# Performance work log

Measured on AMD Instinct MI355X. Metric: run time of the kernel, lower is better.

Reference implementation:

```python
import jax, jax.numpy as jnp
import numpy as np

B = 64
SIZES = [5023, 1256, 314, 79, 20]
NV = [s + 1 for s in SIZES]          # vertex counts incl. padding vertex
K = 12                               # spiral length (all levels)
LAT = 128
ENC_F = [3, 16, 32, 64, 128]
DEC_IN = [128, 64, 32, 32, 16]
DEC_OUT = [64, 32, 32, 16, 3]


def setup_inputs() -> dict:
    keys = iter(jax.random.split(jax.random.key(0), 80))

    def nrm(shape, scale=1.0):
        return jax.random.normal(next(keys), shape, jnp.float32) * scale

    inp = {}
    inp['x_talking'] = nrm((B, NV[0], 3))
    inp['template'] = nrm((B, NV[0], 3))
    for i in range(4):
        inp['D%d' % i] = nrm((NV[i + 1], NV[i]), 1.0 / np.sqrt(NV[i]))
        inp['U%d' % i] = nrm((NV[i], NV[i + 1]), 1.0 / np.sqrt(NV[i + 1]))
    for i in range(4):
        fan = ENC_F[i] * K
        inp['enc_w%d' % i] = nrm((ENC_F[i + 1], fan), 1.0 / np.sqrt(fan))
        inp['enc_b%d' % i] = jnp.zeros((ENC_F[i + 1],), jnp.float32)
    inp['fc_enc_w'] = nrm((LAT, NV[4] * DEC_IN[0]), 1.0 / np.sqrt(NV[4] * DEC_IN[0]))
    inp['fc_enc_b'] = jnp.zeros((LAT,), jnp.float32)
    inp['fc_dec_w'] = nrm((NV[4] * DEC_IN[0], 2 * LAT), 1.0 / np.sqrt(2 * LAT))
    inp['fc_dec_b'] = jnp.zeros((NV[4] * DEC_IN[0],), jnp.float32)
    for i in range(5):
        fan = DEC_IN[i] * K
        inp['dec_w%d' % i] = nrm((DEC_OUT[i], fan), 1.0 / np.sqrt(fan))
        inp['dec_b%d' % i] = jnp.zeros((DEC_OUT[i],), jnp.float32)
    for i in range(4):
        inp['S%d' % i] = jax.random.randint(next(keys), (NV[i], K), 0, NV[i], jnp.int32)
    return inp


def _spiral_conv(x, S, W, b, act):
    # x: [B, N, F]; S: [N, K] spiral neighbor indices; W: [out, K*F] (torch Linear layout)
    Bv, Nv, F = x.shape
    g = x[:, S, :].reshape(Bv, Nv, K * F)            # spiral neighbor gather
    y = act(jnp.einsum('bnf,of->bno', g, W) + b)     # gather-GEMM + activation
    mask = jnp.ones((1, Nv, 1), y.dtype).at[0, -1, 0].set(0.0)  # zero out padding vertex
    return y * mask


def _forward(x_talking, template, D, U, enc, fc_enc_w, fc_enc_b, fc_dec_w, fc_dec_b, dec, S):
    elu = jax.nn.elu
    # encode_talking
    x = x_talking
    for i in range(4):
        x = _spiral_conv(x, S[i], enc[i][0], enc[i][1], elu)
        x = jnp.einsum('mn,bnf->bmf', D[i], x)       # downsample
    z = x.reshape(B, -1) @ fc_enc_w.T + fc_enc_b     # [B, latent]
    # decode(z, z)
    h = jnp.concatenate([z, z], axis=1) @ fc_dec_w.T + fc_dec_b
    x = h.reshape(B, NV[4], DEC_IN[0])
    for i in range(3):
        x = jnp.einsum('mn,bnf->bmf', U[3 - i], x)   # upsample
        x = _spiral_conv(x, S[3 - i], dec[i][0], dec[i][1], elu)
    x = jnp.einsum('mn,bnf->bmf', U[0], x)
    x = _spiral_conv(x, S[0], dec[3][0], dec[3][1], elu)
    x = _spiral_conv(x, S[0], dec[4][0], dec[4][1], lambda v: v)  # identity activation
    return x, x + template


def reference(x_talking, template, D0, D1, D2, D3, U0, U1, U2, U3,
              enc_w0, enc_b0, enc_w1, enc_b1, enc_w2, enc_b2, enc_w3, enc_b3,
              fc_enc_w, fc_enc_b, fc_dec_w, fc_dec_b,
              dec_w0, dec_b0, dec_w1, dec_b1, dec_w2, dec_b2, dec_w3, dec_b3, dec_w4, dec_b4,
              S0, S1, S2, S3):
    return _forward(
        x_talking, template,
        [D0, D1, D2, D3], [U0, U1, U2, U3],
        [(enc_w0, enc_b0), (enc_w1, enc_b1), (enc_w2, enc_b2), (enc_w3, enc_b3)],
        fc_enc_w, fc_enc_b, fc_dec_w, fc_dec_b,
        [(dec_w0, dec_b0), (dec_w1, dec_b1), (dec_w2, dec_b2), (dec_w3, dec_b3), (dec_w4, dec_b4)],
        [S0, S1, S2, S3])
```

## Files before the change

kernel.cpp:

```cpp
#include <hip/hip_runtime.h>
#include <cstddef>


#define BATCH 64
#define SPK 12

typedef __attribute__((ext_vector_type(8))) short bf16x8;
typedef __attribute__((ext_vector_type(4))) short bf16x4;
typedef __attribute__((ext_vector_type(4))) float f32x4;

__device__ __forceinline__ unsigned short f2bf(float x) {
    union { float f; unsigned int u; } v; v.f = x;
    unsigned int r = v.u + 0x7FFF + ((v.u >> 16) & 1);
    return (unsigned short)(r >> 16);
}

__global__ __launch_bounds__(256) void f32_to_bf16_kernel(
    const float* __restrict__ in, unsigned short* __restrict__ out, int n8)
{
    int i = blockIdx.x * 256 + threadIdx.x;
    if (i < n8) {
        const float* p = in + (size_t)i * 8;
        bf16x8 r;
#pragma unroll
        for (int j = 0; j < 8; ++j) r[j] = (short)f2bf(p[j]);
        *(bf16x8*)(out + (size_t)i * 8) = r;
    }
}

__global__ __launch_bounds__(256) void reducep_bf16_kernel(
    const float* __restrict__ P, size_t ps, unsigned short* __restrict__ out,
    int n8, int nparts)
{
    int i = blockIdx.x * 256 + threadIdx.x;
    if (i < n8) {
        size_t base = (size_t)i * 8;
        bf16x8 r;
#pragma unroll
        for (int j = 0; j < 8; ++j) {
            float v = P[base + j];
            for (int p = 1; p < nparts; ++p) v += P[(size_t)p * ps + base + j];
            r[j] = (short)f2bf(v);
        }
        *(bf16x8*)(out + base) = r;
    }
}

__global__ __launch_bounds__(256) void a_bf16_pad_kernel(
    const float* __restrict__ A, unsigned short* __restrict__ Ap,
    int M, int K, int Kp, int total)
{
    int i = blockIdx.x * 256 + threadIdx.x;
    if (i >= total) return;
    int kp8 = Kp >> 3;
    int m = i / kp8;
    int k0 = (i - m * kp8) * 8;
    bf16x8 r;
    if (m < M) {
        const float* src = A + (size_t)m * K + k0;
#pragma unroll
        for (int j = 0; j < 8; ++j) {
            float v = (k0 + j < K) ? src[j] : 0.f;
            r[j] = (short)f2bf(v);
        }
    } else {
#pragma unroll
        for (int j = 0; j < 8; ++j) r[j] = 0;
    }
    *(bf16x8*)(Ap + (size_t)m * Kp + k0) = r;
}

__global__ __launch_bounds__(256) void w_frag16_kernel(
    const unsigned short* __restrict__ Wb, unsigned short* __restrict__ Wfs,
    int KF, int total)
{
    int i = blockIdx.x * 256 + threadIdx.x;
    if (i >= total) return;
    int j    = i & 7;
    int lane = (i >> 3) & 63;
    int s    = i >> 9;
    int l15  = lane & 15;
    int quad = (lane >> 4) & 3;
    Wfs[i] = Wb[l15 * KF + s * 32 + quad * 8 + j];
}

template<int LOGF, int OBF16>
__global__ __launch_bounds__(64, 4) void conv_cmfma_kernel(
    const unsigned short* __restrict__ x, const int* __restrict__ S,
    const unsigned short* __restrict__ Wfs, const float* __restrict__ bias,
    void* __restrict__ yv, int Nv, int elu_flag, int swz)
{
    constexpr int F     = 1 << LOGF;
    constexpr int KF    = SPK * F;
    constexpr int NS    = KF / 32;
    constexpr int RPADu = (LOGF == 5) ? 40 : 24;
    __shared__ unsigned short Gs[12 * 16 * RPADu];

    const int lane = threadIdx.x;
    const int l15  = lane & 15;
    const int quad = (lane >> 4) & 3;

    int bx = blockIdx.x, bz = blockIdx.z;
    if (swz) {
        const int gx = gridDim.x;
        const int total = gx * gridDim.z;
        int bid = bx + gx * bz;
        const int chunk = total >> 3;
        int sid = (bid & 7) * chunk + (bid >> 3);
        bx = sid % gx;
        bz = sid / gx;
    }
    const int n0 = bx * 16;
    const int b  = bz;
    const size_t xb = (size_t)b * Nv;

    int4 sv;
    {
        int g = lane >> 4; if (g > 2) g = 2;
        int n = n0 + l15; if (n >= Nv) n = 0;
        sv = *(const int4*)(S + n * SPK + g * 4);
    }

    if constexpr (LOGF == 5) {
        const int grow = lane >> 2, gchk = lane & 3;
#pragma unroll
        for (int k = 0; k < 12; ++k) {
            int sel = ((k >> 2) << 4) | grow;
            int comp = k & 3;
            int src = (comp == 0) ? __shfl(sv.x, sel)
                    : (comp == 1) ? __shfl(sv.y, sel)
                    : (comp == 2) ? __shfl(sv.z, sel)
                                  : __shfl(sv.w, sel);
            bf16x8 v = *(const bf16x8*)(x + ((xb + src) << 5) + gchk * 8);
            *(bf16x8*)&Gs[k * 16 * RPADu + grow * RPADu + gchk * 8] = v;
        }
    } else {
        const int khalf = lane >> 5, grow = (lane >> 1) & 15, gchk = lane & 1;
#pragma unroll
        for (int g = 0; g < 6; ++g) {
            int k0 = 2 * g;
            int sel0 = ((k0 >> 2) << 4) | grow;
            int sel1 = (((k0 + 1) >> 2) << 4) | grow;
            int s0 = ((k0 & 3) == 0) ? __shfl(sv.x, sel0) : __shfl(sv.z, sel0);
            int s1 = (((k0 + 1) & 3) == 1) ? __shfl(sv.y, sel1) : __shfl(sv.w, sel1);
            int src = khalf ? s1 : s0;
            int k   = k0 + khalf;
            bf16x8 v = *(const bf16x8*)(x + ((xb + src) << 4) + gchk * 8);
            *(bf16x8*)&Gs[k * 16 * RPADu + grow * RPADu + gchk * 8] = v;
        }
    }

    f32x4 acc0 = (f32x4){0.f, 0.f, 0.f, 0.f};
    f32x4 acc1 = (f32x4){0.f, 0.f, 0.f, 0.f};
#pragma unroll
    for (int s = 0; s < NS; ++s) {
        int kf = s * 32 + quad * 8;
        int k  = kf >> LOGF;
        int f  = kf & (F - 1);
        bf16x8 a = *(const bf16x8*)&Gs[k * 16 * RPADu + l15 * RPADu + f];
        bf16x8 w = *(const bf16x8*)(Wfs + (s * 64 + lane) * 8);
        if (s & 1) acc1 = __builtin_amdgcn_mfma_f32_16x16x32_bf16(a, w, acc1, 0, 0, 0);
        else       acc0 = __builtin_amdgcn_mfma_f32_16x16x32_bf16(a, w, acc0, 0, 0, 0);
    }

    float bv = bias[l15];
#pragma unroll
    for (int reg = 0; reg < 4; ++reg) {
        int nn = n0 + quad * 4 + reg;
        if (nn >= Nv) continue;
        float v = acc0[reg] + acc1[reg] + bv;
        if (elu_flag && v <= 0.f) v = expm1f(v);
        if (nn == Nv - 1) v = 0.f;
        size_t off = ((size_t)b * Nv + nn) * 16 + l15;
        if (OBF16) ((unsigned short*)yv)[off] = f2bf(v);
        else       ((float*)yv)[off] = v;
    }
}

template<int LOGF, int OBF16>
__global__ __launch_bounds__(64) void conv_wmfma_kernel(
    const unsigned short* __restrict__ x, const int* __restrict__ S,
    const unsigned short* __restrict__ Wb, const float* __restrict__ bias,
    void* __restrict__ yv, int Nv, int O, int elu_flag, int swz)
{
    constexpr int F  = 1 << LOGF;
    constexpr int KF = SPK * F;
    constexpr int NS = KF / 32;
    const int lane = threadIdx.x;
    const int l15  = lane & 15;
    const int quad = lane >> 4;

    int bx = blockIdx.x, by = blockIdx.y, bz = blockIdx.z;
    if (swz) {
        const int gx = gridDim.x, gy = gridDim.y;
        const int total = gx * gy * gridDim.z;
        int bid = bx + gx * (by + gy * bz);
        const int chunk = total >> 3;
        int sid = (bid & 7) * chunk + (bid >> 3);
        bx = sid % gx; sid /= gx;
        by = sid % gy;
        bz = sid / gy;
    }

    const int n0   = bx * 16;
    const int o    = by * 16 + l15;
    const int b    = bz;
    const size_t xb = (size_t)b * Nv;

    const int n  = n0 + l15;
    const int ng = (n < Nv) ? n : 0;
    const unsigned short* wrow = Wb + (size_t)o * KF;

    f32x4 acc0 = (f32x4){0.f, 0.f, 0.f, 0.f};
    f32x4 acc1 = (f32x4){0.f, 0.f, 0.f, 0.f};
#pragma unroll
    for (int s = 0; s < NS; ++s) {
        int kf  = s * 32 + quad * 8;
        int k   = kf >> LOGF;
        int f   = kf & (F - 1);
        int src = S[ng * SPK + k];
        bf16x8 a = *(const bf16x8*)(x + ((xb + src) << LOGF) + f);
        bf16x8 w = *(const bf16x8*)(wrow + kf);
        if (s & 1) acc1 = __builtin_amdgcn_mfma_f32_16x16x32_bf16(a, w, acc1, 0, 0, 0);
        else       acc0 = __builtin_amdgcn_mfma_f32_16x16x32_bf16(a, w, acc0, 0, 0, 0);
    }
    float bv = bias[o];
#pragma unroll
    for (int reg = 0; reg < 4; ++reg) {
        int nn = n0 + quad * 4 + reg;
        if (nn >= Nv) continue;
        float v = acc0[reg] + acc1[reg] + bv;
        if (elu_flag && v <= 0.f) v = expm1f(v);
        if (nn == Nv - 1) v = 0.f;
        size_t off = ((size_t)b * Nv + nn) * O + o;
        if (OBF16) ((unsigned short*)yv)[off] = f2bf(v);
        else       ((float*)yv)[off] = v;
    }
}

template<int LOGF>
__global__ __launch_bounds__(256) void conv_mfma32_kernel(
    const unsigned short* __restrict__ x, const int* __restrict__ S,
    const unsigned short* __restrict__ Wb, const float* __restrict__ bias,
    float* __restrict__ y, int Nv, int KF, int elu_flag)
{
    constexpr int PAD = 40;
    __shared__ unsigned short Gs[2][256 * PAD];

    const int b    = blockIdx.x;
    const int n0   = blockIdx.y * 256;
    const int tid  = threadIdx.x;
    const int lane = tid & 63;
    const int wave = tid >> 6;
    const int wm   = wave * 64;
    const int l15  = lane & 15;
    const int quad = lane >> 4;
    const size_t xb = (size_t)b * Nv;
    const int nslab = KF >> 5;

    f32x4 acc[4][2];
#pragma unroll
    for (int t = 0; t < 4; ++t)
#pragma unroll
        for (int o = 0; o < 2; ++o) acc[t][o] = (f32x4){0.f, 0.f, 0.f, 0.f};

    auto gath = [&](int k0, bf16x8* g) {
        int n = n0 + tid;
        if (n < Nv) {
#pragma unroll
            for (int j = 0; j < 4; ++j) {
                int kf  = k0 + j * 8;
                int k   = kf >> LOGF;
                int f   = kf & ((1 << LOGF) - 1);
                int src = S[n * SPK + k];
                g[j] = *(const bf16x8*)(x + ((xb + src) << LOGF) + f);
            }
        } else {
#pragma unroll
            for (int j = 0; j < 4; ++j)
#pragma unroll
                for (int e = 0; e < 8; ++e) g[j][e] = 0;
        }
    };
    auto put = [&](int buf, const bf16x8* g) {
#pragma unroll
        for (int j = 0; j < 4; ++j)
            *(bf16x8*)&Gs[buf][tid * PAD + j * 8] = g[j];
    };
    auto wfrag = [&](int k0, int o16) {
        return *(const bf16x8*)(Wb + (size_t)(o16 * 16 + l15) * KF + k0 + quad * 8);
    };

    bf16x8 gcur[4], gnext[4];
    gath(0, gcur);
    put(0, gcur);
    __syncthreads();

    for (int s = 0; s < nslab; ++s) {
        const int cur = s & 1;
        const bool more = (s + 1) < nslab;
        if (more) gath((s + 1) * 32, gnext);
        bf16x8 wf0 = wfrag(s * 32, 0);
        bf16x8 wf1 = wfrag(s * 32, 1);
#pragma unroll
        for (int t = 0; t < 4; ++t) {
            bf16x8 a = *(const bf16x8*)&Gs[cur][(wm + t * 16 + l15) * PAD + quad * 8];
            acc[t][0] = __builtin_amdgcn_mfma_f32_16x16x32_bf16(a, wf0, acc[t][0], 0, 0, 0);
            acc[t][1] = __builtin_amdgcn_mfma_f32_16x16x32_bf16(a, wf1, acc[t][1], 0, 0, 0);
        }
        if (more) {
            put(cur ^ 1, gnext);
            __syncthreads();
        }
    }

    float bv0 = bias[l15];
    float bv1 = bias[16 + l15];
#pragma unroll
    for (int t = 0; t < 4; ++t)
#pragma unroll
        for (int reg = 0; reg < 4; ++reg) {
            int n = n0 + wm + t * 16 + quad * 4 + reg;
            if (n >= Nv) continue;
            float v0 = acc[t][0][reg] + bv0;
            float v1 = acc[t][1][reg] + bv1;
            if (elu_flag) {
                if (v0 <= 0.f) v0 = expm1f(v0);
                if (v1 <= 0.f) v1 = expm1f(v1);
            }
            if (n == Nv - 1) { v0 = 0.f; v1 = 0.f; }
            size_t off = ((size_t)b * Nv + n) * 32 + l15;
            y[off]      = v0;
            y[off + 16] = v1;
        }
}

template<int OBF16>
__global__ __launch_bounds__(256) void dsamp_mfma3_kernel(
    const unsigned short* __restrict__ Ab, const unsigned short* __restrict__ Xt,
    void* __restrict__ Yv, int M, int Kp, int logF, int kchunk,
    int atomic_flag, int swz, size_t pstride)
{
    constexpr int PAD = 40;
    __shared__ unsigned short As[2][128 * PAD];
    __shared__ unsigned short Bs[2][128 * PAD];

    int bx = blockIdx.x, by = blockIdx.y, bz = blockIdx.z;
    if (swz) {
        const int gx = gridDim.x, gy = gridDim.y;
        const int total = gx * gy * gridDim.z;
        int bid = bx + gx * (by + gy * bz);
        const int chunk = total >> 3;
        int sid = (bid & 7) * chunk + (bid >> 3);
        bx = sid % gx; sid /= gx;
        by = sid % gy;
        bz = sid / gy;
    }

    const int fmask = (1 << logF) - 1;
    const int m0   = bx * 128;
    const int c0   = by * 128;
    const int kbeg = bz * kchunk;
    int kend = kbeg + kchunk; if (kend > Kp) kend = Kp;
    const int nslab = (kend - kbeg + 31) >> 5;
    const size_t zoff = (size_t)bz * pstride;

    const int tid  = threadIdx.x;
    const int lane = tid & 63;
    const int wave = tid >> 6;
    const int wm   = (wave >> 1) * 64;
    const int wn   = (wave & 1) * 64;
    const int l15  = lane & 15;
    const int quad = lane >> 4;

    const int s_row = tid >> 2;
    const int s_k8  = (tid & 3) * 8;

    f32x4 acc[4][4];
#pragma unroll
    for (int i = 0; i < 4; ++i)
#pragma unroll
        for (int j = 0; j < 4; ++j) acc[i][j] = (f32x4){0.f, 0.f, 0.f, 0.f};

    bf16x8 apre[2], bpre[2];

    auto loadAB = [&](int ko) {
        apre[0] = *(const bf16x8*)(Ab + (size_t)(m0 + s_row)      * Kp + ko + s_k8);
        apre[1] = *(const bf16x8*)(Ab + (size_t)(m0 + s_row + 64) * Kp + ko + s_k8);
        bpre[0] = *(const bf16x8*)(Xt + (size_t)(c0 + s_row)      * Kp + ko + s_k8);
        bpre[1] = *(const bf16x8*)(Xt + (size_t)(c0 + s_row + 64) * Kp + ko + s_k8);
    };
    auto stage = [&](int buf) {
        *(bf16x8*)&As[buf][s_row * PAD + s_k8]        = apre[0];
        *(bf16x8*)&As[buf][(s_row + 64) * PAD + s_k8] = apre[1];
        *(bf16x8*)&Bs[buf][s_row * PAD + s_k8]        = bpre[0];
        *(bf16x8*)&Bs[buf][(s_row + 64) * PAD + s_k8] = bpre[1];
    };

    loadAB(kbeg);
    stage(0);
    __syncthreads();

    for (int s = 0; s < nslab; ++s) {
        const int cur = s & 1;
        const bool more = (s + 1) < nslab;
        if (more) loadAB(kbeg + (s + 1) * 32);

        bf16x8 af[4], bfr[4];
#pragma unroll
        for (int t = 0; t < 4; ++t) {
            af[t]  = *(const bf16x8*)&As[cur][(wm + t * 16 + l15) * PAD + quad * 8];
            bfr[t] = *(const bf16x8*)&Bs[cur][(wn + t * 16 + l15) * PAD + quad * 8];
        }
#pragma unroll
        for (int tm = 0; tm < 4; ++tm)
#pragma unroll
            for (int tn = 0; tn < 4; ++tn)
                acc[tm][tn] = __builtin_amdgcn_mfma_f32_16x16x32_bf16(af[tm], bfr[tn], acc[tm][tn], 0, 0, 0);

        if (more) { stage(cur ^ 1); __syncthreads(); }
    }

#pragma unroll
    for (int tm = 0; tm < 4; ++tm)
#pragma unroll
        for (int tn = 0; tn < 4; ++tn)
#pragma unroll
            for (int reg = 0; reg < 4; ++reg) {
                int m  = m0 + wm + tm * 16 + quad * 4 + reg;
                int cc = c0 + wn + tn * 16 + l15;
                if (m < M) {
                    int bb = cc >> logF, f = cc & fmask;
                    size_t off = zoff + (((size_t)bb * M + m) << logF) + f;
                    float v = acc[tm][tn][reg];
                    if (OBF16)            ((unsigned short*)Yv)[off] = f2bf(v);
                    else if (atomic_flag) atomicAdd((float*)Yv + off, v);
                    else                  ((float*)Yv)[off] = v;
                }
            }
}

template<int OBF16>
__global__ __launch_bounds__(256) void dsamp_mfma2_kernel(
    const unsigned short* __restrict__ Ap, const float* __restrict__ X,
    void* __restrict__ Yv, int M, int K, int Kp, int logF, int kchunk,
    int atomic_flag, size_t pstride)
{
    constexpr int PAD = 40;
    __shared__ unsigned short Xs[2][64 * PAD];

    const int fmask = (1 << logF) - 1;
    const int m0   = blockIdx.x * 64;
    const int c0   = blockIdx.y * 64;
    const int kbeg = blockIdx.z * kchunk;
    int kend = kbeg + kchunk; if (kend > K) kend = K;
    const int nslab = (kend - kbeg + 31) >> 5;
    const size_t zoff = (size_t)blockIdx.z * pstride;

    const int tid  = threadIdx.x;
    const int lane = tid & 63;
    const int wave = tid >> 6;
    const int wm   = (wave >> 1) * 32;
    const int wn   = (wave & 1) * 32;
    const int l15  = lane & 15;
    const int quad = lane >> 4;

    const int skk  = tid >> 4;
    const int scg  = (tid & 15) * 4;
    const int cB   = c0 + scg;
    const int xbb  = cB >> logF;
    const int xf   = cB & fmask;
    const size_t xrowbase = (((size_t)xbb * K) << logF) + xf;

    const int mA0 = m0 + wm + l15;
    const int mA1 = mA0 + 16;
    const int kaoff = quad * 8;

    f32x4 acc[2][2];
    acc[0][0] = acc[0][1] = acc[1][0] = acc[1][1] = (f32x4){0.f, 0.f, 0.f, 0.f};

    float4 xn0, xn1;
    bf16x8 ac0, ac1, an0, an1;

    {
        int k = kbeg + skk;
        xn0 = make_float4(0.f, 0.f, 0.f, 0.f);
        if (k < kend) xn0 = *(const float4*)(X + xrowbase + ((size_t)k << logF));
        k = kbeg + 16 + skk;
        xn1 = make_float4(0.f, 0.f, 0.f, 0.f);
        if (k < kend) xn1 = *(const float4*)(X + xrowbase + ((size_t)k << logF));
        int ka = kbeg + kaoff;
        ac0 = *(const bf16x8*)(Ap + (size_t)mA0 * Kp + ka);
        ac1 = *(const bf16x8*)(Ap + (size_t)mA1 * Kp + ka);
        unsigned short* p = &Xs[0][0];
        p[(scg + 0) * PAD + skk] = f2bf(xn0.x);
        p[(scg + 1) * PAD + skk] = f2bf(xn0.y);
        p[(scg + 2) * PAD + skk] = f2bf(xn0.z);
        p[(scg + 3) * PAD + skk] = f2bf(xn0.w);
        int kk1 = 16 + skk;
        p[(scg + 0) * PAD + kk1] = f2bf(xn1.x);
        p[(scg + 1) * PAD + kk1] = f2bf(xn1.y);
        p[(scg + 2) * PAD + kk1] = f2bf(xn1.z);
        p[(scg + 3) * PAD + kk1] = f2bf(xn1.w);
    }
    __syncthreads();

    for (int s = 0; s < nslab; ++s) {
        const int cur = s & 1;
        const bool more = (s + 1 < nslab);
        if (more) {
            int k0 = kbeg + (s + 1) * 32;
            int k = k0 + skk;
            xn0 = make_float4(0.f, 0.f, 0.f, 0.f);
            if (k < kend) xn0 = *(const float4*)(X + xrowbase + ((size_t)k << logF));
            k = k0 + 16 + skk;
            xn1 = make_float4(0.f, 0.f, 0.f, 0.f);
            if (k < kend) xn1 = *(const float4*)(X + xrowbase + ((size_t)k << logF));
            int ka = k0 + kaoff;
            an0 = *(const bf16x8*)(Ap + (size_t)mA0 * Kp + ka);
            an1 = *(const bf16x8*)(Ap + (size_t)mA1 * Kp + ka);
        }
        {
            const unsigned short* p = &Xs[cur][0];
            bf16x8 b0 = *(const bf16x8*)&p[(wn +      l15) * PAD + quad * 8];
            bf16x8 b1 = *(const bf16x8*)&p[(wn + 16 + l15) * PAD + quad * 8];
            acc[0][0] = __builtin_amdgcn_mfma_f32_16x16x32_bf16(ac0, b0, acc[0][0], 0, 0, 0);
            acc[0][1] = __builtin_amdgcn_mfma_f32_16x16x32_bf16(ac0, b1, acc[0][1], 0, 0, 0);
            acc[1][0] = __builtin_amdgcn_mfma_f32_16x16x32_bf16(ac1, b0, acc[1][0], 0, 0, 0);
            acc[1][1] = __builtin_amdgcn_mfma_f32_16x16x32_bf16(ac1, b1, acc[1][1], 0, 0, 0);
        }
        if (more) {
            unsigned short* q = &Xs[cur ^ 1][0];
            q[(scg + 0) * PAD + skk] = f2bf(xn0.x);
            q[(scg + 1) * PAD + skk] = f2bf(xn0.y);
            q[(scg + 2) * PAD + skk] = f2bf(xn0.z);
            q[(scg + 3) * PAD + skk] = f2bf(xn0.w);
            int kk1 = 16 + skk;
            q[(scg + 0) * PAD + kk1] = f2bf(xn1.x);
            q[(scg + 1) * PAD + kk1] = f2bf(xn1.y);
            q[(scg + 2) * PAD + kk1] = f2bf(xn1.z);
            q[(scg + 3) * PAD + kk1] = f2bf(xn1.w);
            __syncthreads();
            ac0 = an0; ac1 = an1;
        }
    }

#pragma unroll
    for (int tm = 0; tm < 2; ++tm)
#pragma unroll
        for (int tn = 0; tn < 2; ++tn)
#pragma unroll
            for (int reg = 0; reg < 4; ++reg) {
                int m  = m0 + wm + tm * 16 + quad * 4 + reg;
                int cc = c0 + wn + tn * 16 + l15;
                if (m < M) {
                    int bb = cc >> logF, f = cc & fmask;
                    size_t off = zoff + (((size_t)bb * M + m) << logF) + f;
                    float v = acc[tm][tn][reg];
                    if (OBF16)            ((unsigned short*)Yv)[off] = f2bf(v);
                    else if (atomic_flag) atomicAdd((float*)Yv + off, v);
                    else                  ((float*)Yv)[off] = v;
                }
            }
}

template<int MT, int OT>
__global__ __launch_bounds__(256) void conv_gemm_kernel(
    const float* __restrict__ x, const int* __restrict__ S,
    const float* __restrict__ W, const float* __restrict__ bias,
    float* __restrict__ y, int Nv, int logF, int O, int KF, int KFr,
    int elu_flag)
{
    constexpr int CT = OT / 4;
    constexpr int RT = 256 / CT;
    static_assert(RT * 4 == MT, "tile shape");
    __shared__ float Gs[32][MT];
    __shared__ float Ws[32][OT];

    const int b   = blockIdx.x;
    const int n0  = blockIdx.y * MT;
    const int tid = threadIdx.x;
    const int cx  = tid % CT;
    const int ry  = tid / CT;
    const int r0  = ry * 4;
    const int o0  = cx * 4;
    const int fmask = (1 << logF) - 1;
    const size_t xb = (size_t)b * Nv;

    float acc[4][4];
#pragma unroll
    for (int i = 0; i < 4; ++i)
#pragma unroll
        for (int j = 0; j < 4; ++j) acc[i][j] = 0.f;

    for (int k0 = 0; k0 < KF; k0 += 32) {
        constexpr int GSLOTS = MT * 8;
#pragma unroll
        for (int i = 0; i < GSLOTS / 256; ++i) {
            int idx = tid + i * 256;
            int r   = idx & (MT - 1);
            int jg  = idx / MT;
            int j0  = jg * 4;
            int n   = n0 + r;
            int kf  = k0 + j0;
            float4 v = make_float4(0.f, 0.f, 0.f, 0.f);
            if (n < Nv && kf < KFr) {
                int k   = kf >> logF;
                int f   = kf & fmask;
                int src = S[n * SPK + k];
                v = *(const float4*)(x + ((xb + src) << logF) + f);
            }
            Gs[j0 + 0][r] = v.x; Gs[j0 + 1][r] = v.y;
            Gs[j0 + 2][r] = v.z; Gs[j0 + 3][r] = v.w;
        }
        constexpr int WSLOTS = OT * 8;
#pragma unroll
        for (int i = 0; i < (WSLOTS + 255) / 256; ++i) {
            int idx = tid + i * 256;
            if (WSLOTS >= 256 || idx < WSLOTS) {
                int o  = idx & (OT - 1);
                int jg = idx / OT;
                int j0 = jg * 4;
                float4 v = *(const float4*)(W + (size_t)o * KF + k0 + j0);
                Ws[j0 + 0][o] = v.x; Ws[j0 + 1][o] = v.y;
                Ws[j0 + 2][o] = v.z; Ws[j0 + 3][o] = v.w;
            }
        }
        __syncthreads();
#pragma unroll
        for (int kk = 0; kk < 32; ++kk) {
            float4 g = *(const float4*)&Gs[kk][r0];
            float4 w = *(const float4*)&Ws[kk][o0];
            acc[0][0] += g.x * w.x; acc[0][1] += g.x * w.y; acc[0][2] += g.x * w.z; acc[0][3] += g.x * w.w;
            acc[1][0] += g.y * w.x; acc[1][1] += g.y * w.y; acc[1][2] += g.y * w.z; acc[1][3] += g.y * w.w;
            acc[2][0] += g.z * w.x; acc[2][1] += g.z * w.y; acc[2][2] += g.z * w.z; acc[2][3] += g.z * w.w;
            acc[3][0] += g.w * w.x; acc[3][1] += g.w * w.y; acc[3][2] += g.w * w.z; acc[3][3] += g.w * w.w;
        }
        __syncthreads();
    }

    float4 bv = *(const float4*)(bias + o0);
#pragma unroll
    for (int i = 0; i < 4; ++i) {
        int n = n0 + r0 + i;
        if (n >= Nv) continue;
        float v0 = acc[i][0] + bv.x;
        float v1 = acc[i][1] + bv.y;
        float v2 = acc[i][2] + bv.z;
        float v3 = acc[i][3] + bv.w;
        if (elu_flag) {
            v0 = v0 > 0.f ? v0 : expm1f(v0);
            v1 = v1 > 0.f ? v1 : expm1f(v1);
            v2 = v2 > 0.f ? v2 : expm1f(v2);
            v3 = v3 > 0.f ? v3 : expm1f(v3);
        }
        if (n == Nv - 1) { v0 = v1 = v2 = v3 = 0.f; }
        *(float4*)(y + ((size_t)b * Nv + n) * O + o0) = make_float4(v0, v1, v2, v3);
    }
}

template<int OBF16>
__global__ __launch_bounds__(256) void dsamp_kernel(
    const float* __restrict__ A, const float* __restrict__ X,
    void* __restrict__ Yv, int M, int N, int F)
{
    __shared__ float As[16][68];
    __shared__ float Xs[16][64];

    const int m0  = blockIdx.x * 64;
    const int c0  = blockIdx.y * 64;
    const int tid = threadIdx.x;
    const int tx  = tid & 15;
    const int ty  = tid >> 4;

    float acc[4][4];
#pragma unroll
    for (int i = 0; i < 4; ++i)
#pragma unroll
        for (int j = 0; j < 4; ++j) acc[i][j] = 0.f;

    for (int k0 = 0; k0 < N; k0 += 16) {
#pragma unroll
        for (int p = 0; p < 4; ++p) {
            int r  = (tid >> 4) + p * 16;
            int kk = tid & 15;
            int m  = m0 + r;
            int n  = k0 + kk;
            float v = 0.f;
            if (m < M && n < N) v = A[(size_t)m * N + n];
            As[kk][r] = v;
        }
        {
            int kk = tid >> 4;
            int cc = (tid & 15) * 4;
            int n  = k0 + kk;
            float4 v = make_float4(0.f, 0.f, 0.f, 0.f);
            if (n < N) {
                int c  = c0 + cc;
                int bb = c / F;
                int f  = c - bb * F;
                v = *(const float4*)(X + ((size_t)bb * N + n) * F + f);
            }
            *(float4*)&Xs[kk][cc] = v;
        }
        __syncthreads();
#pragma unroll
        for (int kk = 0; kk < 16; ++kk) {
            float4 av = *(const float4*)&As[kk][ty * 4];
            float4 xv = *(const float4*)&Xs[kk][tx * 4];
            acc[0][0] += av.x * xv.x; acc[0][1] += av.x * xv.y; acc[0][2] += av.x * xv.z; acc[0][3] += av.x * xv.w;
            acc[1][0] += av.y * xv.x; acc[1][1] += av.y * xv.y; acc[1][2] += av.y * xv.z; acc[1][3] += av.y * xv.w;
            acc[2][0] += av.z * xv.x; acc[2][1] += av.z * xv.y; acc[2][2] += av.z * xv.z; acc[2][3] += av.z * xv.w;
            acc[3][0] += av.w * xv.x; acc[3][1] += av.w * xv.y; acc[3][2] += av.w * xv.z; acc[3][3] += av.w * xv.w;
        }
        __syncthreads();
    }

    const int cbase = c0 + tx * 4;
    const int bb = cbase / F;
    const int f  = cbase - bb * F;
#pragma unroll
    for (int i = 0; i < 4; ++i) {
        int m = m0 + ty * 4 + i;
        if (m < M) {
            size_t off = ((size_t)bb * M + m) * F + f;
            if (OBF16) {
                bf16x4 v;
                v[0] = (short)f2bf(acc[i][0]); v[1] = (short)f2bf(acc[i][1]);
                v[2] = (short)f2bf(acc[i][2]); v[3] = (short)f2bf(acc[i][3]);
                *(bf16x4*)((unsigned short*)Yv + off) = v;
            } else {
                *(float4*)((float*)Yv + off) =
                    make_float4(acc[i][0], acc[i][1], acc[i][2], acc[i][3]);
            }
        }
    }
}

__global__ __launch_bounds__(256) void fc_wave_kernel(
    const float* __restrict__ in, const float* __restrict__ W,
    const float* __restrict__ bias, float* __restrict__ out,
    int In, int O, int dup)
{
    const int gw   = blockIdx.x * 4 + (threadIdx.x >> 6);
    const int lane = threadIdx.x & 63;
    const int b = gw / O;
    const int o = gw - b * O;
    const float* xr = in + (size_t)b * In;
    float acc = 0.f;
    if (dup) {
        const float* wr = W + (size_t)o * (2 * In);
        for (int k = lane; k < In; k += 64)
            acc += xr[k] * (wr[k] + wr[In + k]);
    } else {
        const float* wr = W + (size_t)o * In;
        for (int k = lane; k < In; k += 64)
            acc += xr[k] * wr[k];
    }
#pragma unroll
    for (int off = 32; off > 0; off >>= 1)
        acc += __shfl_down(acc, off, 64);
    if (lane == 0) out[(size_t)b * O + o] = acc + bias[o];
}

__global__ __launch_bounds__(256) void xpose_bf16_kernel(
    const float* __restrict__ x, unsigned short* __restrict__ xt,
    int K, int Kp, int logF)
{
    const int c  = blockIdx.y * 256 + threadIdx.x;
    const int k0 = blockIdx.x * 8;
    const int bb = c >> logF;
    const int f  = c & ((1 << logF) - 1);
    const float* src = x + (((size_t)bb * K) << logF) + f;
    bf16x8 r;
#pragma unroll
    for (int j = 0; j < 8; ++j) {
        int k = k0 + j;
        float v = (k < K) ? src[(size_t)k << logF] : 0.f;
        r[j] = (short)f2bf(v);
    }
    *(bf16x8*)(xt + (size_t)c * Kp + k0) = r;
}

__global__ __launch_bounds__(256) void pad_e0_w_kernel(
    const float* __restrict__ w, float* __restrict__ wp)
{
    int i = blockIdx.x * 256 + threadIdx.x;
    if (i < 1024) {
        int o = i >> 6, kf = i & 63;
        int k = kf >> 2, f = kf & 3;
        wp[i] = (f < 3 && k < 12) ? w[o * 36 + k * 3 + f] : 0.f;
    }
}
__global__ __launch_bounds__(256) void pad_x4_kernel(
    const float* __restrict__ x, float* __restrict__ xp, int n)
{
    int i = blockIdx.x * 256 + threadIdx.x;
    if (i < n) {
        int f = i & 3, nb = i >> 2;
        xp[i] = (f < 3) ? x[nb * 3 + f] : 0.f;
    }
}
__global__ __launch_bounds__(256) void pad_c4_w_kernel(
    const float* __restrict__ w, const float* __restrict__ b,
    float* __restrict__ wp, float* __restrict__ bp)
{
    int i = blockIdx.x * 256 + threadIdx.x;
    if (i < 3072) {
        int o = i / 192;
        wp[i] = (o < 3) ? w[i] : 0.f;
    }
    if (i < 16) bp[i] = (i < 3) ? b[i] : 0.f;
}
__global__ __launch_bounds__(256) void extract_add_kernel(
    const float* __restrict__ cp, const float* __restrict__ t,
    float* __restrict__ o0, float* __restrict__ o1, int n)
{
    int i = blockIdx.x * 256 + threadIdx.x;
    if (i < n) {
        int f = i % 3, nb = i / 3;
        float v = cp[(size_t)nb * 16 + f];
        o0[i] = v;
        o1[i] = v + t[i];
    }
}


static inline int ilog2(int v) { int l = 0; while ((1 << l) < v) ++l; return l; }

static inline void a_bf16_launch(const float* A, unsigned short* Ap, int M, int K,
                                 int Mp, int Kp, hipStream_t s)
{
    int total = Mp * (Kp >> 3);
    a_bf16_pad_kernel<<<(total + 255) / 256, 256, 0, s>>>(A, Ap, M, K, Kp, total);
}

template<int OBF16>
static inline void dsamp_mfma2_launch(const unsigned short* Ap, const float* X,
                                      void* Y, int M, int K, int Kp, int F,
                                      int ks, int partial, hipStream_t s)
{
    int kchunk = (K + ks - 1) / ks;
    kchunk = (kchunk + 31) & ~31;
    int ksz = (K + kchunk - 1) / kchunk;
    int atomic = (ksz > 1 && !partial) ? 1 : 0;
    size_t pstride = (partial && ksz > 1) ? (size_t)BATCH * M * F : 0;
    dim3 grid((M + 63) / 64, F, ksz);
    dsamp_mfma2_kernel<OBF16><<<grid, 256, 0, s>>>(Ap, X, Y, M, K, Kp, ilog2(F),
                                                   kchunk, atomic, pstride);
}

template<int OBF16>
static inline void dsamp_mfma3_launch(const unsigned short* Ab, const unsigned short* Xt,
                                      void* Y, int M, int Kp, int F,
                                      int ks, int partial, hipStream_t s)
{
    int slabs = Kp >> 5;
    int kchunk = ((slabs + ks - 1) / ks) * 32;
    int ksz = (Kp + kchunk - 1) / kchunk;
    int gx = (M + 127) / 128, gy = (BATCH * F) / 128;
    int total = gx * gy * ksz;
    int swz = ((total & 7) == 0) ? 1 : 0;
    int atomic = (ksz > 1 && !partial) ? 1 : 0;
    size_t pstride = (partial && ksz > 1) ? (size_t)BATCH * M * F : 0;
    dim3 grid(gx, gy, ksz);
    dsamp_mfma3_kernel<OBF16><<<grid, 256, 0, s>>>(Ab, Xt, Y, M, Kp, ilog2(F),
                                                   kchunk, atomic, swz, pstride);
}

template<int OBF16>
static inline void dsamp_launch(const float* A, const float* X, void* Y,
                                int M, int N, int F, hipStream_t s)
{
    dim3 grid((M + 63) / 64, F);
    dsamp_kernel<OBF16><<<grid, 256, 0, s>>>(A, X, Y, M, N, F);
}

extern "C" void kernel_launch(void* const* d_in, const int* in_sizes, int n_in,
                              void* d_out, int out_size, void* d_ws, size_t ws_size,
                              hipStream_t stream)
{
    const float* x_talking = (const float*)d_in[0];
    const float* templ     = (const float*)d_in[1];
    const float* D0 = (const float*)d_in[2];
    const float* U0 = (const float*)d_in[3];
    const float* D1 = (const float*)d_in[4];
    const float* U1 = (const float*)d_in[5];
    const float* D2 = (const float*)d_in[6];
    const float* U2 = (const float*)d_in[7];
    const float* D3 = (const float*)d_in[8];
    const float* U3 = (const float*)d_in[9];
    const float* enc_w0 = (const float*)d_in[10]; const float* enc_b0 = (const float*)d_in[11];
    const float* enc_w1 = (const float*)d_in[12]; const float* enc_b1 = (const float*)d_in[13];
    const float* enc_w2 = (const float*)d_in[14]; const float* enc_b2 = (const float*)d_in[15];
    const float* enc_w3 = (const float*)d_in[16]; const float* enc_b3 = (const float*)d_in[17];
    const float* fc_enc_w = (const float*)d_in[18]; const float* fc_enc_b = (const float*)d_in[19];
    const float* fc_dec_w = (const float*)d_in[20]; const float* fc_dec_b = (const float*)d_in[21];
    const float* dec_w0 = (const float*)d_in[22]; const float* dec_b0 = (const float*)d_in[23];
    const float* dec_w1 = (const float*)d_in[24]; const float* dec_b1 = (const float*)d_in[25];
    const float* dec_w2 = (const float*)d_in[26]; const float* dec_b2 = (const float*)d_in[27];
    const float* dec_w3 = (const float*)d_in[28]; const float* dec_b3 = (const float*)d_in[29];
    const float* dec_w4 = (const float*)d_in[30]; const float* dec_b4 = (const float*)d_in[31];
    const int* S0 = (const int*)d_in[32];
    const int* S1 = (const int*)d_in[33];
    const int* S2 = (const int*)d_in[34];
    const int* S3 = (const int*)d_in[35];

    float* bufA = (float*)d_ws;
    float* bufB = bufA + 10289152;

    float* out0 = (float*)d_out;
    float* out1 = out0 + 964608;

    unsigned short* Xt_e0 = (unsigned short*)(bufB + 1290240);
    unsigned short* Xt_c2 = (unsigned short*)bufB;
    unsigned short* U0b   = (unsigned short*)(bufB + 1400000);
    unsigned short* Wb_e2 = (unsigned short*)(bufB + 4700000);
    unsigned short* Wb_e3 = (unsigned short*)(bufB + 4715000);
    unsigned short* Wb_c0 = (unsigned short*)(bufB + 4765000);
    unsigned short* Wb_c1 = (unsigned short*)(bufB + 4815000);
    unsigned short* D2b   = (unsigned short*)(bufB + 4830000);
    unsigned short* U2b   = (unsigned short*)(bufB + 4860000);
    float* xpad   = bufA + 5200000;
    float* WpE0   = bufA + 6600000;
    unsigned short* D0b   = (unsigned short*)(bufA + 6700000);
    unsigned short* D1b   = (unsigned short*)(bufA + 9950000);
    unsigned short* U1b   = (unsigned short*)(bufA + 4000000);
    unsigned short* Wb_e1 = (unsigned short*)(bufA + 10160000);
    unsigned short* Wb_c2 = (unsigned short*)(bufA + 10170000);
    float*          Pd0   = bufA;
    unsigned short* Xb_e1 = (unsigned short*)bufB;
    float*          Pd1   = bufA + 5200000;
    unsigned short* Xb_e2   = (unsigned short*)(bufA + 2000000);
    float*          Pd2   = bufB;
    unsigned short* Xb_e3   = (unsigned short*)(bufA + 2000000);
    unsigned short* Xb_c2in = (unsigned short*)(bufA + 2600000);
    unsigned short* Xb_c3n  = (unsigned short*)bufA;
    unsigned short* Xb_c4   = (unsigned short*)(bufA + 5200000);
    unsigned short* Wb_c3  = (unsigned short*)(bufA + 7800000);
    unsigned short* Wfs_c3 = (unsigned short*)(bufA + 7805000);
    float* WpC4   = bufA + 7810000;
    float* BpC4   = bufA + 7813500;
    unsigned short* Wb_c4  = (unsigned short*)(bufA + 7814000);
    unsigned short* Wfs_c4 = (unsigned short*)(bufA + 7818000);

    pad_e0_w_kernel<<<4, 256, 0, stream>>>(enc_w0, WpE0);
    pad_x4_kernel<<<5024, 256, 0, stream>>>(x_talking, xpad, 1286144);
    a_bf16_launch(D0, D0b, 1257, 5024, 1280, 5024, stream);
    a_bf16_launch(D1, D1b, 315, 1257, 320, 1280, stream);
    a_bf16_launch(D2, D2b, 80, 315, 128, 320, stream);
    a_bf16_launch(U2, U2b, 315, 80, 320, 96, stream);
    f32_to_bf16_kernel<<<3, 256, 0, stream>>>(enc_w1, Wb_e1, 768);
    f32_to_bf16_kernel<<<6, 256, 0, stream>>>(dec_w2, Wb_c2, 1536);
    f32_to_bf16_kernel<<<12, 256, 0, stream>>>(enc_w2, Wb_e2, 3072);
    f32_to_bf16_kernel<<<48, 256, 0, stream>>>(enc_w3, Wb_e3, 12288);
    f32_to_bf16_kernel<<<48, 256, 0, stream>>>(dec_w0, Wb_c0, 12288);
    f32_to_bf16_kernel<<<12, 256, 0, stream>>>(dec_w1, Wb_c1, 3072);

    {
        dim3 grid(BATCH, (5024 + 255) / 256);
        conv_gemm_kernel<256, 16><<<grid, 256, 0, stream>>>(
            xpad, S0, WpE0, enc_b0, bufA, 5024, 2, 16, 64, 48, 1);
    }
    xpose_bf16_kernel<<<dim3(628, 4), 256, 0, stream>>>(bufA, Xt_e0, 5024, 5024, 4);
    dsamp_mfma3_launch<0>(D0b, Xt_e0, Pd0, 1257, 5024, 16, 5, 1, stream);
    reducep_bf16_kernel<<<629, 256, 0, stream>>>(Pd0, 1287168, Xb_e1, 160896, 5);
    a_bf16_launch(U0, U0b, 5024, 1257, 5120, 1280, stream);
    a_bf16_launch(U1, U1b, 1257, 315, 1280, 320, stream);
    {
        dim3 grid(BATCH, (1257 + 255) / 256);
        conv_mfma32_kernel<4><<<grid, 256, 0, stream>>>(
            Xb_e1, S1, Wb_e1, enc_b1, bufA, 1257, 192, 1);
    }
    dsamp_mfma2_launch<0>(D1b, bufA, Pd1, 315, 1257, 1280, 32, 4, 1, stream);
    reducep_bf16_kernel<<<315, 256, 0, stream>>>(Pd1, 645120, Xb_e2, 80640, 4);
    {
        dim3 grid((315 + 15) / 16, 64 / 16, BATCH);
        conv_wmfma_kernel<5, 0><<<grid, 64, 0, stream>>>(
            Xb_e2, S2, Wb_e2, enc_b2, bufA, 315, 64, 1, 0);
    }
    dsamp_mfma2_launch<0>(D2b, bufA, Pd2, 80, 315, 320, 64, 4, 1, stream);
    reducep_bf16_kernel<<<160, 256, 0, stream>>>(Pd2, 327680, Xb_e3, 40960, 4);
    {
        dim3 grid((80 + 15) / 16, 128 / 16, BATCH);
        conv_wmfma_kernel<6, 0><<<grid, 64, 0, stream>>>(
            Xb_e3, S3, Wb_e3, enc_b3, bufA, 80, 128, 1, 0);
    }
    dsamp_launch<0>(D3, bufA, bufB, 21, 80, 128, stream);

    fc_wave_kernel<<<dim3((BATCH * 128) / 4), 256, 0, stream>>>(bufB, fc_enc_w, fc_enc_b, bufA, 2688, 128, 0);
    fc_wave_kernel<<<dim3((BATCH * 2688) / 4), 256, 0, stream>>>(bufA, fc_dec_w, fc_dec_b, bufB, 128, 2688, 1);

    dsamp_launch<1>(U3, bufB, bufA, 80, 21, 128, stream);
    {
        dim3 grid((80 + 15) / 16, 64 / 16, BATCH);
        conv_wmfma_kernel<7, 0><<<grid, 64, 0, stream>>>(
            (const unsigned short*)bufA, S3, Wb_c0, dec_b0, bufB, 80, 64, 1, 0);
    }
    dsamp_mfma2_launch<1>(U2b, bufB, bufA, 315, 80, 96, 64, 1, 0, stream);
    {
        dim3 grid((315 + 15) / 16, 32 / 16, BATCH);
        conv_wmfma_kernel<6, 0><<<grid, 64, 0, stream>>>(
            (const unsigned short*)bufA, S2, Wb_c1, dec_b1, bufB, 315, 32, 1, 0);
    }
    dsamp_mfma2_launch<1>(U1b, bufB, Xb_c2in, 1257, 315, 320, 32, 1, 0, stream);
    {
        dim3 grid(BATCH, (1257 + 255) / 256);
        conv_mfma32_kernel<5><<<grid, 256, 0, stream>>>(
            Xb_c2in, S1, Wb_c2, dec_b2, bufA, 1257, 384, 1);
    }
    xpose_bf16_kernel<<<dim3(160, 8), 256, 0, stream>>>(bufA, Xt_c2, 1257, 1280, 5);
    dsamp_mfma3_launch<1>(U0b, Xt_c2, Xb_c3n, 5024, 1280, 32, 1, 0, stream);

    f32_to_bf16_kernel<<<3, 256, 0, stream>>>(dec_w3, Wb_c3, 768);
    w_frag16_kernel<<<24, 256, 0, stream>>>(Wb_c3, Wfs_c3, 384, 6144);
    pad_c4_w_kernel<<<12, 256, 0, stream>>>(dec_w4, dec_b4, WpC4, BpC4);
    f32_to_bf16_kernel<<<2, 256, 0, stream>>>(WpC4, Wb_c4, 384);
    w_frag16_kernel<<<12, 256, 0, stream>>>(Wb_c4, Wfs_c4, 192, 3072);
    {
        dim3 grid(5024 / 16, 1, BATCH);
        conv_cmfma_kernel<5, 1><<<grid, 64, 0, stream>>>(
            Xb_c3n, S0, Wfs_c3, dec_b3, (void*)Xb_c4, 5024, 1, 1);
    }
    {
        dim3 grid(5024 / 16, 1, BATCH);
        conv_cmfma_kernel<4, 0><<<grid, 64, 0, stream>>>(
            Xb_c4, S0, Wfs_c4, BpC4, (void*)bufB, 5024, 0, 1);
    }
    extract_add_kernel<<<(964608 + 255) / 256, 256, 0, stream>>>(bufB, templ, out0, out1, 964608);
}
```

Measured before the change: 647.0 us.

## Merge weight prep launches into one kernel and use nontemporal partial-sum traffic

Replaces about a dozen small weight conversion, padding and fragment-reordering kernels with a single prep_weights_kernel that writes every bf16, padded and fragment-layout weight buffer in one launch. This removes per-launch overhead and the intermediate Wb_c3, WpC4 and Wb_c4 buffers. It also makes the split-K partial-sum stores in the downsample GEMMs and the loads in the reduction kernel nontemporal, to reduce cache pollution from these streaming buffers. The buffer offsets for the weight scratch areas move within bufA, so they must not overlap live activation regions.

```diff
diff --git a/kernel.cpp b/kernel.cpp
--- a/kernel.cpp
+++ b/kernel.cpp
@@ -15,18 +15,55 @@
     return (unsigned short)(r >> 16);
 }
 
-__global__ __launch_bounds__(256) void f32_to_bf16_kernel(
-    const float* __restrict__ in, unsigned short* __restrict__ out, int n8)
+__global__ __launch_bounds__(256) void prep_weights_kernel(
+    const float* __restrict__ enc_w0, const float* __restrict__ enc_w1,
+    const float* __restrict__ enc_w2, const float* __restrict__ enc_w3,
+    const float* __restrict__ dec_w0, const float* __restrict__ dec_w1,
+    const float* __restrict__ dec_w2, const float* __restrict__ dec_w3,
+    const float* __restrict__ dec_w4, const float* __restrict__ dec_b4,
+    float* __restrict__ WpE0, unsigned short* __restrict__ Wb_e1,
+    unsigned short* __restrict__ Wb_c2, unsigned short* __restrict__ Wb_e2,
+    unsigned short* __restrict__ Wb_e3, unsigned short* __restrict__ Wb_c0,
+    unsigned short* __restrict__ Wb_c1, unsigned short* __restrict__ Wfs_c3,
+    unsigned short* __restrict__ Wfs_c4, float* __restrict__ BpC4)
 {
     int i = blockIdx.x * 256 + threadIdx.x;
-    if (i < n8) {
-        const float* p = in + (size_t)i * 8;
-        bf16x8 r;
-#pragma unroll
-        for (int j = 0; j < 8; ++j) r[j] = (short)f2bf(p[j]);
-        *(bf16x8*)(out + (size_t)i * 8) = r;
-    }
-}
+    if (i < 1024) {
+        int o = i >> 6, kf = i & 63, k = kf >> 2, f = kf & 3;
+        WpE0[i] = (f < 3 && k < 12) ? enc_w0[o * 36 + k * 3 + f] : 0.f;
+        return;
+    }
+    i -= 1024;
+    if (i < 6144)  { Wb_e1[i] = f2bf(enc_w1[i]); return; }
+    i -= 6144;
+    if (i < 12288) { Wb_c2[i] = f2bf(dec_w2[i]); return; }
+    i -= 12288;
+    if (i < 24576) { Wb_e2[i] = f2bf(enc_w2[i]); return; }
+    i -= 24576;
+    if (i < 98304) { Wb_e3[i] = f2bf(enc_w3[i]); return; }
+    i -= 98304;
+    if (i < 98304) { Wb_c0[i] = f2bf(dec_w0[i]); return; }
+    i -= 98304;
+    if (i < 24576) { Wb_c1[i] = f2bf(dec_w1[i]); return; }
+    i -= 24576;
+    if (i < 6144) {
+        int j = i & 7, lane = (i >> 3) & 63, s = i >> 9;
+        int l15 = lane & 15, quad = (lane >> 4) & 3;
+        Wfs_c3[i] = f2bf(dec_w3[l15 * 384 + s * 32 + quad * 8 + j]);
+        return;
+    }
+    i -= 6144;
+    if (i < 3072) {
+        int j = i & 7, lane = (i >> 3) & 63, s = i >> 9;
+        int l15 = lane & 15, quad = (lane >> 4) & 3;
+        Wfs_c4[i] = (l15 < 3) ? f2bf(dec_w4[l15 * 192 + s * 32 + quad * 8 + j])
+                              : (unsigned short)0;
+        return;
+    }
+    i -= 3072;
+    if (i < 16) BpC4[i] = (i < 3) ? dec_b4[i] : 0.f;
+}
+#define PREP_TOTAL (1024 + 6144 + 12288 + 24576 + 98304 + 98304 + 24576 + 6144 + 3072 + 16)
 
 __global__ __launch_bounds__(256) void reducep_bf16_kernel(
     const float* __restrict__ P, size_t ps, unsigned short* __restrict__ out,
@@ -38,8 +75,9 @@
         bf16x8 r;
 #pragma unroll
         for (int j = 0; j < 8; ++j) {
-            float v = P[base + j];
-            for (int p = 1; p < nparts; ++p) v += P[(size_t)p * ps + base + j];
+            float v = __builtin_nontemporal_load(&P[base + j]);
+            for (int p = 1; p < nparts; ++p)
+                v += __builtin_nontemporal_load(&P[(size_t)p * ps + base + j]);
             r[j] = (short)f2bf(v);
         }
         *(bf16x8*)(out + base) = r;
@@ -68,20 +106,6 @@
         for (int j = 0; j < 8; ++j) r[j] = 0;
     }
     *(bf16x8*)(Ap + (size_t)m * Kp + k0) = r;
-}
-
-__global__ __launch_bounds__(256) void w_frag16_kernel(
-    const unsigned short* __restrict__ Wb, unsigned short* __restrict__ Wfs,
-    int KF, int total)
-{
-    int i = blockIdx.x * 256 + threadIdx.x;
-    if (i >= total) return;
-    int j    = i & 7;
-    int lane = (i >> 3) & 63;
-    int s    = i >> 9;
-    int l15  = lane & 15;
-    int quad = (lane >> 4) & 3;
-    Wfs[i] = Wb[l15 * KF + s * 32 + quad * 8 + j];
 }
 
 template<int LOGF, int OBF16>
@@ -335,7 +359,7 @@
         }
 }
 
-template<int OBF16>
+template<int OBF16, int NT>
 __global__ __launch_bounds__(256) void dsamp_mfma3_kernel(
     const unsigned short* __restrict__ Ab, const unsigned short* __restrict__ Xt,
     void* __restrict__ Yv, int M, int Kp, int logF, int kchunk,
@@ -435,12 +459,13 @@
                     float v = acc[tm][tn][reg];
                     if (OBF16)            ((unsigned short*)Yv)[off] = f2bf(v);
                     else if (atomic_flag) atomicAdd((float*)Yv + off, v);
+                    else if (NT)          __builtin_nontemporal_store(v, (float*)Yv + off);
                     else                  ((float*)Yv)[off] = v;
                 }
             }
 }
 
-template<int OBF16>
+template<int OBF16, int NT>
 __global__ __launch_bounds__(256) void dsamp_mfma2_kernel(
     const unsigned short* __restrict__ Ap, const float* __restrict__ X,
     void* __restrict__ Yv, int M, int K, int Kp, int logF, int kchunk,
@@ -559,6 +584,7 @@
                     float v = acc[tm][tn][reg];
                     if (OBF16)            ((unsigned short*)Yv)[off] = f2bf(v);
                     else if (atomic_flag) atomicAdd((float*)Yv + off, v);
+                    else if (NT)          __builtin_nontemporal_store(v, (float*)Yv + off);
                     else                  ((float*)Yv)[off] = v;
                 }
             }
@@ -782,16 +808,6 @@
     *(bf16x8*)(xt + (size_t)c * Kp + k0) = r;
 }
 
-__global__ __launch_bounds__(256) void pad_e0_w_kernel(
-    const float* __restrict__ w, float* __restrict__ wp)
-{
-    int i = blockIdx.x * 256 + threadIdx.x;
-    if (i < 1024) {
-        int o = i >> 6, kf = i & 63;
-        int k = kf >> 2, f = kf & 3;
-        wp[i] = (f < 3 && k < 12) ? w[o * 36 + k * 3 + f] : 0.f;
-    }
-}
 __global__ __launch_bounds__(256) void pad_x4_kernel(
     const float* __restrict__ x, float* __restrict__ xp, int n)
 {
@@ -800,17 +816,6 @@
         int f = i & 3, nb = i >> 2;
         xp[i] = (f < 3) ? x[nb * 3 + f] : 0.f;
     }
-}
-__global__ __launch_bounds__(256) void pad_c4_w_kernel(
-    const float* __restrict__ w, const float* __restrict__ b,
-    float* __restrict__ wp, float* __restrict__ bp)
-{
-    int i = blockIdx.x * 256 + threadIdx.x;
-    if (i < 3072) {
-        int o = i / 192;
-        wp[i] = (o < 3) ? w[i] : 0.f;
-    }
-    if (i < 16) bp[i] = (i < 3) ? b[i] : 0.f;
 }
 __global__ __launch_bounds__(256) void extract_add_kernel(
     const float* __restrict__ cp, const float* __restrict__ t,
@@ -835,7 +840,7 @@
     a_bf16_pad_kernel<<<(total + 255) / 256, 256, 0, s>>>(A, Ap, M, K, Kp, total);
 }
 
-template<int OBF16>
+template<int OBF16, int NT>
 static inline void dsamp_mfma2_launch(const unsigned short* Ap, const float* X,
                                       void* Y, int M, int K, int Kp, int F,
                                       int ks, int partial, hipStream_t s)
@@ -846,11 +851,11 @@
     int atomic = (ksz > 1 && !partial) ? 1 : 0;
     size_t pstride = (partial && ksz > 1) ? (size_t)BATCH * M * F : 0;
     dim3 grid((M + 63) / 64, F, ksz);
-    dsamp_mfma2_kernel<OBF16><<<grid, 256, 0, s>>>(Ap, X, Y, M, K, Kp, ilog2(F),
-                                                   kchunk, atomic, pstride);
-}
-
-template<int OBF16>
+    dsamp_mfma2_kernel<OBF16, NT><<<grid, 256, 0, s>>>(Ap, X, Y, M, K, Kp, ilog2(F),
+                                                       kchunk, atomic, pstride);
+}
+
+template<int OBF16, int NT>
 static inline void dsamp_mfma3_launch(const unsigned short* Ab, const unsigned short* Xt,
                                       void* Y, int M, int Kp, int F,
                                       int ks, int partial, hipStream_t s)
@@ -864,8 +869,8 @@
     int atomic = (ksz > 1 && !partial) ? 1 : 0;
     size_t pstride = (partial && ksz > 1) ? (size_t)BATCH * M * F : 0;
     dim3 grid(gx, gy, ksz);
-    dsamp_mfma3_kernel<OBF16><<<grid, 256, 0, s>>>(Ab, Xt, Y, M, Kp, ilog2(F),
-                                                   kchunk, atomic, swz, pstride);
+    dsamp_mfma3_kernel<OBF16, NT><<<grid, 256, 0, s>>>(Ab, Xt, Y, M, Kp, ilog2(F),
+                                                       kchunk, atomic, swz, pstride);
 }
 
 template<int OBF16>
@@ -922,12 +927,15 @@
     unsigned short* D2b   = (unsigned short*)(bufB + 4830000);
     unsigned short* U2b   = (unsigned short*)(bufB + 4860000);
     float* xpad   = bufA + 5200000;
-    float* WpE0   = bufA + 6600000;
     unsigned short* D0b   = (unsigned short*)(bufA + 6700000);
     unsigned short* D1b   = (unsigned short*)(bufA + 9950000);
     unsigned short* U1b   = (unsigned short*)(bufA + 4000000);
     unsigned short* Wb_e1 = (unsigned short*)(bufA + 10160000);
     unsigned short* Wb_c2 = (unsigned short*)(bufA + 10170000);
+    unsigned short* Wfs_c3 = (unsigned short*)(bufA + 10180000);
+    unsigned short* Wfs_c4 = (unsigned short*)(bufA + 10185000);
+    float* BpC4   = bufA + 10190000;
+    float* WpE0   = bufA + 10195000;
     float*          Pd0   = bufA;
     unsigned short* Xb_e1 = (unsigned short*)bufB;
     float*          Pd1   = bufA + 5200000;
@@ -937,25 +945,16 @@
     unsigned short* Xb_c2in = (unsigned short*)(bufA + 2600000);
     unsigned short* Xb_c3n  = (unsigned short*)bufA;
     unsigned short* Xb_c4   = (unsigned short*)(bufA + 5200000);
-    unsigned short* Wb_c3  = (unsigned short*)(bufA + 7800000);
-    unsigned short* Wfs_c3 = (unsigned short*)(bufA + 7805000);
-    float* WpC4   = bufA + 7810000;
-    float* BpC4   = bufA + 7813500;
-    unsigned short* Wb_c4  = (unsigned short*)(bufA + 7814000);
-    unsigned short* Wfs_c4 = (unsigned short*)(bufA + 7818000);
-
-    pad_e0_w_kernel<<<4, 256, 0, stream>>>(enc_w0, WpE0);
+
+    prep_weights_kernel<<<(PREP_TOTAL + 255) / 256, 256, 0, stream>>>(
+        enc_w0, enc_w1, enc_w2, enc_w3, dec_w0, dec_w1, dec_w2, dec_w3,
+        dec_w4, dec_b4, WpE0, Wb_e1, Wb_c2, Wb_e2, Wb_e3, Wb_c0, Wb_c1,
+        Wfs_c3, Wfs_c4, BpC4);
     pad_x4_kernel<<<5024, 256, 0, stream>>>(x_talking, xpad, 1286144);
     a_bf16_launch(D0, D0b, 1257, 5024, 1280, 5024, stream);
     a_bf16_launch(D1, D1b, 315, 1257, 320, 1280, stream);
     a_bf16_launch(D2, D2b, 80, 315, 128, 320, stream);
     a_bf16_launch(U2, U2b, 315, 80, 320, 96, stream);
-    f32_to_bf16_kernel<<<3, 256, 0, stream>>>(enc_w1, Wb_e1, 768);
-    f32_to_bf16_kernel<<<6, 256, 0, stream>>>(dec_w2, Wb_c2, 1536);
-    f32_to_bf16_kernel<<<12, 256, 0, stream>>>(enc_w2, Wb_e2, 3072);
-    f32_to_bf16_kernel<<<48, 256, 0, stream>>>(enc_w3, Wb_e3, 12288);
-    f32_to_bf16_kernel<<<48, 256, 0, stream>>>(dec_w0, Wb_c0, 12288);
-    f32_to_bf16_kernel<<<12, 256, 0, stream>>>(dec_w1, Wb_c1, 3072);
 
     {
         dim3 grid(BATCH, (5024 + 255) / 256);
@@ -963,7 +962,7 @@
             xpad, S0, WpE0, enc_b0, bufA, 5024, 2, 16, 64, 48, 1);
     }
     xpose_bf16_kernel<<<dim3(628, 4), 256, 0, stream>>>(bufA, Xt_e0, 5024, 5024, 4);
-    dsamp_mfma3_launch<0>(D0b, Xt_e0, Pd0, 1257, 5024, 16, 5, 1, stream);
+    dsamp_mfma3_launch<0, 1>(D0b, Xt_e0, Pd0, 1257, 5024, 16, 5, 1, stream);
     reducep_bf16_kernel<<<629, 256, 0, stream>>>(Pd0, 1287168, Xb_e1, 160896, 5);
     a_bf16_launch(U0, U0b, 5024, 1257, 5120, 1280, stream);
     a_bf16_launch(U1, U1b, 1257, 315, 1280, 320, stream);
@@ -972,14 +971,14 @@
         conv_mfma32_kernel<4><<<grid, 256, 0, stream>>>(
             Xb_e1, S1, Wb_e1, enc_b1, bufA, 1257, 192, 1);
     }
-    dsamp_mfma2_launch<0>(D1b, bufA, Pd1, 315, 1257, 1280, 32, 4, 1, stream);
+    dsamp_mfma2_launch<0, 1>(D1b, bufA, Pd1, 315, 1257, 1280, 32, 4, 1, stream);
     reducep_bf16_kernel<<<315, 256, 0, stream>>>(Pd1, 645120, Xb_e2, 80640, 4);
     {
         dim3 grid((315 + 15) / 16, 64 / 16, BATCH);
         conv_wmfma_kernel<5, 0><<<grid, 64, 0, stream>>>(
             Xb_e2, S2, Wb_e2, enc_b2, bufA, 315, 64, 1, 0);
     }
-    dsamp_mfma2_launch<0>(D2b, bufA, Pd2, 80, 315, 320, 64, 4, 1, stream);
+    dsamp_mfma2_launch<0, 1>(D2b, bufA, Pd2, 80, 315, 320, 64, 4, 1, stream);
     reducep_bf16_kernel<<<160, 256, 0, stream>>>(Pd2, 327680, Xb_e3, 40960, 4);
     {
         dim3 grid((80 + 15) / 16, 128 / 16, BATCH);
@@ -997,26 +996,21 @@
         conv_wmfma_kernel<7, 0><<<grid, 64, 0, stream>>>(
             (const unsigned short*)bufA, S3, Wb_c0, dec_b0, bufB, 80, 64, 1, 0);
     }
-    dsamp_mfma2_launch<1>(U2b, bufB, bufA, 315, 80, 96, 64, 1, 0, stream);
+    dsamp_mfma2_launch<1, 0>(U2b, bufB, bufA, 315, 80, 96, 64, 1, 0, stream);
     {
         dim3 grid((315 + 15) / 16, 32 / 16, BATCH);
         conv_wmfma_kernel<6, 0><<<grid, 64, 0, stream>>>(
             (const unsigned short*)bufA, S2, Wb_c1, dec_b1, bufB, 315, 32, 1, 0);
     }
-    dsamp_mfma2_launch<1>(U1b, bufB, Xb_c2in, 1257, 315, 320, 32, 1, 0, stream);
+    dsamp_mfma2_launch<1, 0>(U1b, bufB, Xb_c2in, 1257, 315, 320, 32, 1, 0, stream);
     {
         dim3 grid(BATCH, (1257 + 255) / 256);
         conv_mfma32_kernel<5><<<grid, 256, 0, stream>>>(
             Xb_c2in, S1, Wb_c2, dec_b2, bufA, 1257, 384, 1);
     }
     xpose_bf16_kernel<<<dim3(160, 8), 256, 0, stream>>>(bufA, Xt_c2, 1257, 1280, 5);
-    dsamp_mfma3_launch<1>(U0b, Xt_c2, Xb_c3n, 5024, 1280, 32, 1, 0, stream);
-
-    f32_to_bf16_kernel<<<3, 256, 0, stream>>>(dec_w3, Wb_c3, 768);
-    w_frag16_kernel<<<24, 256, 0, stream>>>(Wb_c3, Wfs_c3, 384, 6144);
-    pad_c4_w_kernel<<<12, 256, 0, stream>>>(dec_w4, dec_b4, WpC4, BpC4);
-    f32_to_bf16_kernel<<<2, 256, 0, stream>>>(WpC4, Wb_c4, 384);
-    w_frag16_kernel<<<12, 256, 0, stream>>>(Wb_c4, Wfs_c4, 192, 3072);
+    dsamp_mfma3_launch<1, 0>(U0b, Xt_c2, Xb_c3n, 5024, 1280, 32, 1, 0, stream);
+
     {
         dim3 grid(5024 / 16, 1, BATCH);
         conv_cmfma_kernel<5, 1><<<grid, 64, 0, stream>>>(
```

Measured after the change: 648.5 us. About the same (+0.2%).
